# Optimization experiments

Hardware: AMD Instinct MI355X
Metric: run time of the kernel (lower is better)

## Reference

```python
import jax, jax.numpy as jnp
import numpy as np
from jax import lax

MAX_LEN = 40
SOS_ID = 2
VOCAB, EMB, HID, CTX = 32000, 512, 1024, 64
H2 = HID // 2
B, S = 256, 128


def gru_cell(x, h, wih, whh, bih, bhh):
    # PyTorch GRU equations: gates ordered (r, z, n)
    gx = x @ wih.T + bih
    gh = h @ whh.T + bhh
    rx, zx, nx = jnp.split(gx, 3, axis=-1)
    rh, zh, nh = jnp.split(gh, 3, axis=-1)
    r = jax.nn.sigmoid(rx + rh)
    z = jax.nn.sigmoid(zx + zh)
    n = jnp.tanh(nx + r * nh)
    return (1.0 - z) * n + z * h


def setup_inputs() -> dict:
    key = jax.random.key(0)
    ks = jax.random.split(key, 16)
    sd = 0.02
    emb_table = jax.random.normal(ks[0], (VOCAB, EMB), jnp.float32) * sd
    emb_table = emb_table.at[0].set(0.0)  # padding_idx=0
    def w(k, shape):
        return jax.random.normal(k, shape, jnp.float32) * sd
    inp = {
        "input_ids": jax.random.randint(ks[1], (B, S), 0, VOCAB),
        "context_vec": jax.random.normal(ks[2], (B, CTX), jnp.float32),
        "emb_table": emb_table,
        # encoder fwd direction
        "enc_wih_f": w(ks[3], (3 * H2, EMB)),
        "enc_whh_f": w(ks[4], (3 * H2, H2)),
        "enc_bih_f": w(ks[5], (3 * H2,)),
        "enc_bhh_f": w(ks[6], (3 * H2,)),
        # encoder bwd direction
        "enc_wih_b": w(ks[7], (3 * H2, EMB)),
        "enc_whh_b": w(ks[8], (3 * H2, H2)),
        "enc_bih_b": w(ks[9], (3 * H2,)),
        "enc_bhh_b": w(ks[10], (3 * H2,)),
        # decoder GRU: input = emb + hidden + context
        "dec_wih": w(ks[11], (3 * HID, EMB + HID + CTX)),
        "dec_whh": w(ks[12], (3 * HID, HID)),
        "dec_bih": w(ks[13], (3 * HID,)),
        "dec_bhh": w(ks[14], (3 * HID,)),
        "wout": w(ks[15], (VOCAB, HID)),
        "bout": jnp.zeros((VOCAB,), jnp.float32),
    }
    return inp


def reference(input_ids, context_vec, emb_table,
              enc_wih_f, enc_whh_f, enc_bih_f, enc_bhh_f,
              enc_wih_b, enc_whh_b, enc_bih_b, enc_bhh_b,
              dec_wih, dec_whh, dec_bih, dec_bhh, wout, bout):
    b = input_ids.shape[0]
    emb = emb_table[input_ids]                      # [B,S,E]
    emb_t = jnp.swapaxes(emb, 0, 1)                 # [S,B,E]

    def enc_f(h, x):
        return gru_cell(x, h, enc_wih_f, enc_whh_f, enc_bih_f, enc_bhh_f), None

    def enc_b(h, x):
        return gru_cell(x, h, enc_wih_b, enc_whh_b, enc_bih_b, enc_bhh_b), None

    h0 = jnp.zeros((b, H2), emb.dtype)
    hf, _ = lax.scan(enc_f, h0, emb_t)
    hb, _ = lax.scan(enc_b, h0, emb_t[::-1])
    # replicate torch's h_n.view(batch, -1) on a (2,B,H2) tensor (contiguous reshape)
    encoder_ctx = jnp.stack([hf, hb], axis=0).reshape(b, HID)   # [B,HID]

    ctx = jnp.concatenate([encoder_ctx, context_vec], axis=-1)  # [B,HID+CTX]
    h_dec0 = jnp.zeros((b, HID), emb.dtype)
    prev0 = jnp.full((b,), SOS_ID, dtype=jnp.int32)

    def dec_step(carry, _):
        h, prev = carry
        x = jnp.concatenate([emb_table[prev], ctx], axis=-1)
        h = gru_cell(x, h, dec_wih, dec_whh, dec_bih, dec_bhh)
        logits = h @ wout.T + bout                  # [B,V]
        probs = jax.nn.softmax(logits, axis=-1)
        nxt = jnp.argmax(probs, axis=-1).astype(jnp.int32)
        sel = jnp.take_along_axis(probs, nxt[:, None], axis=1)[:, 0]
        lp = jnp.log(sel + 1e-12)
        return (h, nxt), (nxt, lp)

    (_, _), (toks, lps) = lax.scan(dec_step, (h_dec0, prev0), None, length=MAX_LEN)
    return toks.T, lps.T   # [B,MAX_LEN] tokens, [B,MAX_LEN] log-probs
```

## Files before the change

kernel.cpp:

```cpp
#include <hip/hip_runtime.h>
#include <hip/hip_bf16.h>
#include <math.h>

#define B_    256
#define S_    128
#define EMB_  512
#define H2_   512
#define HID_  1024
#define CTX_  64
#define VOC_  32000
#define TMAX_ 40
#define SOS_  2

typedef unsigned short u16;
typedef __attribute__((ext_vector_type(8))) short short8;
typedef __attribute__((ext_vector_type(4))) float f32x4;

__device__ __forceinline__ float4 ld4(const float* p) {
    return *reinterpret_cast<const float4*>(p);
}
__device__ __forceinline__ float sigmoidf_(float x) { return 1.f / (1.f + expf(-x)); }
__device__ __forceinline__ u16 f2bf(float x) {
    union { float f; unsigned int u; } v; v.f = x;
    unsigned int r = v.u + 0x7FFFu + ((v.u >> 16) & 1u);
    return (u16)(r >> 16);
}
__device__ __forceinline__ unsigned pk2(float a, float b) {
    float2 t; t.x = a; t.y = b;
    __hip_bfloat162 h = __float22bfloat162_rn(t);
    return *reinterpret_cast<unsigned*>(&h);
}
__device__ __forceinline__ void merge_top2(float& v1, int& i1, float& v2, int& i2,
                                           float ov1, int oi1, float ov2, int oi2)
{
    if (ov1 > v1 || (ov1 == v1 && oi1 < i1)) {
        float tv = v1; int ti = i1;
        v1 = ov1; i1 = oi1;
        if (ov2 > tv || (ov2 == tv && oi2 < ti)) { v2 = ov2; i2 = oi2; }
        else                                     { v2 = tv;  i2 = ti;  }
    } else {
        if (ov1 > v2 || (ov1 == v2 && oi1 < i2)) { v2 = ov1; i2 = oi1; }
    }
}

template<int BM, int BN, int TM, int TN, int AMODE, int BGATHER, int BIASM>
__launch_bounds__(256)
__global__ void gemm_nt(const float* __restrict__ Ap,
                        const int*   __restrict__ ids,
                        const float* __restrict__ Ex,
                        const float* __restrict__ Bp, int ldb, int bofs,
                        const float* __restrict__ bias,
                        const float* __restrict__ addsrc,
                        float* __restrict__ Cp, int ldc,
                        int lda, int K, int s_base, int sdir)
{
    constexpr int BK = 32;
    __shared__ float As[BK][BM + 4];
    __shared__ float Bs[BK][BN + 4];
    const int t  = threadIdx.x;
    const int tx = t & 15, ty = t >> 4;
    const int m_base = blockIdx.y * BM;
    const int n_base = blockIdx.x * BN;

    float acc[TM][TN];
#pragma unroll
    for (int i = 0; i < TM; ++i)
#pragma unroll
        for (int j = 0; j < TN; ++j) acc[i][j] = 0.f;

    constexpr int A_PER = BM * BK / 4 / 256;
    constexpr int B_PER = BN * BK / 4 / 256;

    for (int k0 = 0; k0 < K; k0 += BK) {
#pragma unroll
        for (int j = 0; j < A_PER; ++j) {
            int f   = t + j * 256;
            int row = f >> 3;
            int kk  = (f & 7) << 2;
            int m   = m_base + row;
            float4 v;
            if constexpr (AMODE == 0) {
                v = ld4(Ap + (size_t)m * lda + k0 + kk);
            } else if constexpr (AMODE == 3) {
                int id = ids[m];
                v = ld4(Ex + (size_t)id * EMB_ + k0 + kk);
            } else {
                int k = k0 + kk;
                if (k < HID_) v = ld4(Ap + (size_t)m * HID_ + k);
                else          v = ld4(Ex + (size_t)m * CTX_ + (k - HID_));
            }
            As[kk + 0][row] = v.x; As[kk + 1][row] = v.y;
            As[kk + 2][row] = v.z; As[kk + 3][row] = v.w;
        }
#pragma unroll
        for (int j = 0; j < B_PER; ++j) {
            int f   = t + j * 256;
            int row = f >> 3;
            int kk  = (f & 7) << 2;
            float4 v;
            if constexpr (BGATHER == 1) {
                int n = n_base + row;
                int s = n >> 8, b = n & 255;
                int id = ids[b * S_ + s_base + sdir * s];
                v = ld4(Ex + (size_t)id * EMB_ + k0 + kk);
            } else {
                v = ld4(Bp + (size_t)(n_base + row) * ldb + bofs + k0 + kk);
            }
            Bs[kk + 0][row] = v.x; Bs[kk + 1][row] = v.y;
            Bs[kk + 2][row] = v.z; Bs[kk + 3][row] = v.w;
        }
        __syncthreads();
#pragma unroll
        for (int kk = 0; kk < BK; ++kk) {
            float a[TM], b[TN];
            *(float4*)&a[0] = ld4(&As[kk][ty * TM]);
            if constexpr (TM == 8) *(float4*)&a[4] = ld4(&As[kk][ty * TM + 4]);
            *(float4*)&b[0] = ld4(&Bs[kk][tx * TN]);
            if constexpr (TN == 8) *(float4*)&b[4] = ld4(&Bs[kk][tx * TN + 4]);
#pragma unroll
            for (int i = 0; i < TM; ++i)
#pragma unroll
                for (int j = 0; j < TN; ++j) acc[i][j] += a[i] * b[j];
        }
        __syncthreads();
    }
#pragma unroll
    for (int i = 0; i < TM; ++i) {
        int m = m_base + ty * TM + i;
#pragma unroll
        for (int j = 0; j < TN; ++j) {
            int n = n_base + tx * TN + j;
            float v = acc[i][j];
            if (bias) v += BIASM ? bias[m] : bias[n];
            if (addsrc) v += addsrc[(size_t)m * ldc + n];
            Cp[(size_t)m * ldc + n] = v;
        }
    }
}

__global__ void whh_trans(const float* __restrict__ whh_f, const float* __restrict__ whh_b,
                          float* __restrict__ whhX_f, float* __restrict__ whhX_b)
{
    int idx = blockIdx.x * 256 + threadIdx.x;
    const float* src = blockIdx.y ? whh_b : whh_f;
    float*       dst = blockIdx.y ? whhX_b : whhX_f;
    int k  = idx / 1536;
    int cc = idx - k * 1536;
    int u  = cc / 3;
    int g  = cc - u * 3;
    dst[idx] = src[(size_t)(g * 512 + u) * 512 + k];
}

#define RECBLK 128

union EncSM {
    struct { float hbuf[2][512][4]; float red[256][25]; } rec;
    struct { float As[32][132]; float Bs[32][132]; } gx;
};

__launch_bounds__(512)
__global__ void enc_fused(const float* __restrict__ grec_f, const float* __restrict__ grec_b,
                          float* __restrict__ gout_f, float* __restrict__ gout_b,
                          const float* __restrict__ whhX_f, const float* __restrict__ whhX_b,
                          const float* __restrict__ bhh_f, const float* __restrict__ bhh_b,
                          const float* __restrict__ wih_f, const float* __restrict__ wih_b,
                          const float* __restrict__ bih_f, const float* __restrict__ bih_b,
                          const int* __restrict__ ids, const float* __restrict__ emb,
                          float* __restrict__ hT, int do_rec, int gx_chunk, int nsteps)
{
    __shared__ __align__(16) EncSM sm;
    const int t = threadIdx.x;

    if (blockIdx.x >= RECBLK) {
        if (gx_chunk < 0) return;
        const int tt  = blockIdx.x - RECBLK;
        const int dz  = tt >= 192;
        const int t192 = dz ? tt - 192 : tt;
        const int m_base = (t192 & 15) * 128;
        const int n_base = (t192 >> 4) * 128;
        const float* W    = dz ? wih_b : wih_f;
        const float* bias = dz ? bih_b : bih_f;
        float*       Cp   = dz ? gout_b : gout_f;
        const int s_base  = dz ? (127 - 8 * gx_chunk) : (8 * gx_chunk);
        const int sdir    = dz ? -1 : 1;
        const int tx = t & 31, ty = t >> 5;

        float acc[8][4];
#pragma unroll
        for (int i = 0; i < 8; ++i)
#pragma unroll
            for (int j = 0; j < 4; ++j) acc[i][j] = 0.f;

        for (int k0 = 0; k0 < 512; k0 += 32) {
#pragma unroll
            for (int j = 0; j < 2; ++j) {
                int f   = t + j * 512;
                int row = f >> 3;
                int kk  = (f & 7) << 2;
                int m   = m_base + row;
                int s   = m >> 8, b = m & 255;
                int id  = ids[b * S_ + s_base + sdir * s];
                float4 v = ld4(emb + (size_t)id * EMB_ + k0 + kk);
                sm.gx.As[kk + 0][row] = v.x; sm.gx.As[kk + 1][row] = v.y;
                sm.gx.As[kk + 2][row] = v.z; sm.gx.As[kk + 3][row] = v.w;
                float4 wv = ld4(W + (size_t)(n_base + row) * 512 + k0 + kk);
                sm.gx.Bs[kk + 0][row] = wv.x; sm.gx.Bs[kk + 1][row] = wv.y;
                sm.gx.Bs[kk + 2][row] = wv.z; sm.gx.Bs[kk + 3][row] = wv.w;
            }
            __syncthreads();
#pragma unroll
            for (int kk = 0; kk < 32; ++kk) {
                float a[8], b[4];
                *(float4*)&a[0] = ld4(&sm.gx.As[kk][ty * 8]);
                *(float4*)&a[4] = ld4(&sm.gx.As[kk][ty * 8 + 4]);
                *(float4*)&b[0] = ld4(&sm.gx.Bs[kk][tx * 4]);
#pragma unroll
                for (int i = 0; i < 8; ++i)
#pragma unroll
                    for (int j = 0; j < 4; ++j) acc[i][j] += a[i] * b[j];
            }
            __syncthreads();
        }
#pragma unroll
        for (int i = 0; i < 8; ++i) {
            int m = m_base + ty * 8 + i;
#pragma unroll
            for (int j = 0; j < 4; ++j) {
                int n = n_base + tx * 4 + j;
                Cp[(size_t)m * 1536 + n] = acc[i][j] + bias[n];
            }
        }
        return;
    }

    if (!do_rec) return;
    const int bid = blockIdx.x;
    const int xcd = bid & 7;
    const int dir = xcd >> 2;
    const int local = (bid >> 3) * 4 + (xcd & 3);
    const int r0 = local * 4;
    const float* gx  = dir ? grec_b : grec_f;
    const float* whx = dir ? whhX_b : whhX_f;
    const float* bhh = dir ? bhh_b : bhh_f;
    float* hTd = hT + (size_t)dir * (256 * 512);

    const int kh = t >> 8;
    const int tu = t & 255;
    const int k_base = kh << 8;

    for (int i = t; i < 2048; i += 512) {
        int r = i >> 9, u = i & 511;
        sm.rec.hbuf[0][u][r] = hTd[(size_t)(r0 + r) * 512 + u];
    }
    float bh[2][3];
#pragma unroll
    for (int uu = 0; uu < 2; ++uu)
#pragma unroll
        for (int g = 0; g < 3; ++g)
            bh[uu][g] = bhh[g * 512 + tu * 2 + uu];
    __syncthreads();

    for (int st = 0; st < nsteps; ++st) {
        const int cur = st & 1, nxt = cur ^ 1;

        float2 gxv[3][4];
        if (!kh) {
#pragma unroll
            for (int g = 0; g < 3; ++g)
#pragma unroll
                for (int r = 0; r < 4; ++r)
                    gxv[g][r] = *(const float2*)&gx[(size_t)((st << 8) + r0 + r) * 1536
                                                    + (g << 9) + (tu << 1)];
        }

        float acc[2][3][4];
#pragma unroll
        for (int uu = 0; uu < 2; ++uu)
#pragma unroll
            for (int g = 0; g < 3; ++g)
#pragma unroll
                for (int r = 0; r < 4; ++r) acc[uu][g][r] = 0.f;

        const float* wp = whx + (size_t)k_base * 1536 + tu * 6;
#pragma unroll 4
        for (int kk = 0; kk < 256; ++kk) {
            float4 hv = *(const float4*)&sm.rec.hbuf[cur][k_base + kk][0];
            float2 w0 = *(const float2*)(wp + 0);
            float2 w1 = *(const float2*)(wp + 2);
            float2 w2 = *(const float2*)(wp + 4);
            const float* hvp = (const float*)&hv;
#pragma unroll
            for (int r = 0; r < 4; ++r) {
                float h = hvp[r];
                acc[0][0][r] += w0.x * h;
                acc[0][1][r] += w0.y * h;
                acc[0][2][r] += w1.x * h;
                acc[1][0][r] += w1.y * h;
                acc[1][1][r] += w2.x * h;
                acc[1][2][r] += w2.y * h;
            }
            wp += 1536;
        }

        if (kh) {
#pragma unroll
            for (int uu = 0; uu < 2; ++uu)
#pragma unroll
                for (int g = 0; g < 3; ++g)
#pragma unroll
                    for (int r = 0; r < 4; ++r)
                        sm.rec.red[tu][(uu * 3 + g) * 4 + r] = acc[uu][g][r];
        }
        __syncthreads();
        if (!kh) {
#pragma unroll
            for (int uu = 0; uu < 2; ++uu)
#pragma unroll
                for (int g = 0; g < 3; ++g)
#pragma unroll
                    for (int r = 0; r < 4; ++r)
                        acc[uu][g][r] += sm.rec.red[tu][(uu * 3 + g) * 4 + r];
#pragma unroll
            for (int uu = 0; uu < 2; ++uu) {
                int u = tu * 2 + uu;
#pragma unroll
                for (int r = 0; r < 4; ++r) {
                    float gr = uu ? gxv[0][r].y : gxv[0][r].x;
                    float gz = uu ? gxv[1][r].y : gxv[1][r].x;
                    float gn = uu ? gxv[2][r].y : gxv[2][r].x;
                    float hold = sm.rec.hbuf[cur][u][r];
                    float rg = sigmoidf_(gr + acc[uu][0][r] + bh[uu][0]);
                    float zg = sigmoidf_(gz + acc[uu][1][r] + bh[uu][1]);
                    float ng = tanhf(gn + rg * (acc[uu][2][r] + bh[uu][2]));
                    sm.rec.hbuf[nxt][u][r] = (1.f - zg) * ng + zg * hold;
                }
            }
        }
        __syncthreads();
    }

    const int lb = nsteps & 1;
    for (int i = t; i < 2048; i += 512) {
        int r = i >> 9, u = i & 511;
        hTd[(size_t)(r0 + r) * 512 + u] = sm.rec.hbuf[lb][u][r];
    }
}

__global__ void zerof(float* __restrict__ p, int n)
{
    int i = blockIdx.x * 256 + threadIdx.x;
    if (i < n) p[i] = 0.f;
}

__global__ void init_dec(float* __restrict__ hdec, u16* __restrict__ hbf, int* __restrict__ prev)
{
    int i = blockIdx.x * 256 + threadIdx.x;
    hdec[i] = 0.f; hbf[i] = 0;
    if (i < B_) prev[i] = SOS_;
}

__global__ void hcat_build(const float* __restrict__ hT, float* __restrict__ hcat)
{
    int idx = blockIdx.x * 256 + threadIdx.x;
    int b = idx >> 10, k = idx & 1023;
    int d = b >> 7;
    int rr = ((2 * b) & 255) + (k >> 9);
    int kk = k & 511;
    hcat[idx] = hT[(size_t)d * 131072 + (size_t)rr * 512 + kk];
}

__launch_bounds__(256)
__global__ void dec_gemm2(const float* __restrict__ hdec, const int* __restrict__ prev,
                          const float* __restrict__ emb,
                          const float* __restrict__ dwhh, const float* __restrict__ dwih,
                          const float* __restrict__ dbhh, const float* __restrict__ gctx,
                          float* __restrict__ ghbuf, float* __restrict__ gibuf)
{
    constexpr int BK = 32;
    __shared__ float As[BK][68];
    __shared__ float Bs[BK][68];
    const int t  = threadIdx.x;
    const int tx = t & 15, ty = t >> 4;
    const bool isH = blockIdx.y < 4;
    const int m_base = (isH ? blockIdx.y : (blockIdx.y - 4)) * 64;
    const int n_base = blockIdx.x * 64;
    const int K   = isH ? 1024 : 512;
    const float* Bp = isH ? dwhh : dwih;
    const int ldb  = isH ? 1024 : 1600;
    float* Cp = isH ? ghbuf : gibuf;

    float acc[4][4];
#pragma unroll
    for (int i = 0; i < 4; ++i)
#pragma unroll
        for (int j = 0; j < 4; ++j) acc[i][j] = 0.f;

    for (int k0 = 0; k0 < K; k0 += BK) {
#pragma unroll
        for (int j = 0; j < 2; ++j) {
            int f   = t + j * 256;
            int row = f >> 3;
            int kk  = (f & 7) << 2;
            int m   = m_base + row;
            float4 v;
            if (isH) v = ld4(hdec + (size_t)m * HID_ + k0 + kk);
            else     v = ld4(emb + (size_t)prev[m] * EMB_ + k0 + kk);
            As[kk + 0][row] = v.x; As[kk + 1][row] = v.y;
            As[kk + 2][row] = v.z; As[kk + 3][row] = v.w;
            float4 w = ld4(Bp + (size_t)(n_base + row) * ldb + k0 + kk);
            Bs[kk + 0][row] = w.x; Bs[kk + 1][row] = w.y;
            Bs[kk + 2][row] = w.z; Bs[kk + 3][row] = w.w;
        }
        __syncthreads();
#pragma unroll
        for (int kk = 0; kk < BK; ++kk) {
            float a[4], b[4];
            *(float4*)&a[0] = ld4(&As[kk][ty * 4]);
            *(float4*)&b[0] = ld4(&Bs[kk][tx * 4]);
#pragma unroll
            for (int i = 0; i < 4; ++i)
#pragma unroll
                for (int j = 0; j < 4; ++j) acc[i][j] += a[i] * b[j];
        }
        __syncthreads();
    }
#pragma unroll
    for (int i = 0; i < 4; ++i) {
        int m = m_base + ty * 4 + i;
#pragma unroll
        for (int j = 0; j < 4; ++j) {
            int n = n_base + tx * 4 + j;
            float v = acc[i][j];
            if (isH) v += dbhh[n];
            else     v += gctx[(size_t)m * 3072 + n];
            Cp[(size_t)m * 3072 + n] = v;
        }
    }
}

__global__ void dec_combine(const float* __restrict__ gi, const float* __restrict__ gh,
                            float* __restrict__ hdec, u16* __restrict__ hbf)
{
    int idx = blockIdx.x * 256 + threadIdx.x;
    int b = idx >> 10, u = idx & 1023;
    size_t gb = (size_t)b * 3072;
    float r = sigmoidf_(gi[gb + u]            + gh[gb + u]);
    float z = sigmoidf_(gi[gb + HID_ + u]     + gh[gb + HID_ + u]);
    float n = tanhf    (gi[gb + 2 * HID_ + u] + r * gh[gb + 2 * HID_ + u]);
    float v = (1.f - z) * n + z * hdec[idx];
    hdec[idx] = v;
    hbf[idx] = f2bf(v);
}

__launch_bounds__(512)
__global__ void gemm_logits(const u16* __restrict__ A, const float* __restrict__ Wf,
                            const float* __restrict__ bias,
                            float* __restrict__ pmax, float* __restrict__ psum,
                            float* __restrict__ ptv, int* __restrict__ pti)
{
    __shared__ u16 As[256][72];
    __shared__ u16 Bs[128][72];
    const int t = threadIdx.x;
    const int lane = t & 63, wave = t >> 6;
    const int wm = (wave & 3) * 64, wn = (wave >> 2) * 64;
    const int n0 = blockIdx.x * 128;
    f32x4 acc[4][4];
#pragma unroll
    for (int i = 0; i < 4; ++i)
#pragma unroll
        for (int j = 0; j < 4; ++j) acc[i][j] = (f32x4){0.f, 0.f, 0.f, 0.f};
    const int arow = t >> 1, aoff = (t & 1) * 32;
    const int brow = t >> 2, boff = (t & 3) * 16;

    for (int k0 = 0; k0 < 1024; k0 += 64) {
#pragma unroll
        for (int q = 0; q < 4; ++q) {
            *(uint4*)&As[arow][aoff + q * 8] =
                *(const uint4*)(A + (size_t)arow * 1024 + k0 + aoff + q * 8);
        }
        const float* wr = Wf + (size_t)(n0 + brow) * 1024 + k0 + boff;
#pragma unroll
        for (int q = 0; q < 2; ++q) {
            float4 x = ld4(wr + q * 8);
            float4 y = ld4(wr + q * 8 + 4);
            uint4 o;
            o.x = pk2(x.x, x.y); o.y = pk2(x.z, x.w);
            o.z = pk2(y.x, y.y); o.w = pk2(y.z, y.w);
            *(uint4*)&Bs[brow][boff + q * 8] = o;
        }
        __syncthreads();
#pragma unroll
        for (int s = 0; s < 2; ++s) {
            short8 a[4], b[4];
            int j0 = s * 32 + (lane >> 4) * 8;
#pragma unroll
            for (int i = 0; i < 4; ++i) {
                a[i] = *(const short8*)&As[wm + i * 16 + (lane & 15)][j0];
                b[i] = *(const short8*)&Bs[wn + i * 16 + (lane & 15)][j0];
            }
#pragma unroll
            for (int i = 0; i < 4; ++i)
#pragma unroll
                for (int j = 0; j < 4; ++j)
                    acc[i][j] = __builtin_amdgcn_mfma_f32_16x16x32_bf16(a[i], b[j], acc[i][j], 0, 0, 0);
        }
        __syncthreads();
    }

    const int htile = blockIdx.x * 2 + (wn >> 6);
    float bn[4]; int jx[4];
#pragma unroll
    for (int j = 0; j < 4; ++j) { jx[j] = n0 + wn + j * 16 + (lane & 15); bn[j] = bias[jx[j]]; }
#pragma unroll
    for (int i = 0; i < 4; ++i) {
#pragma unroll
        for (int rr = 0; rr < 4; ++rr) {
            float v[4];
#pragma unroll
            for (int j = 0; j < 4; ++j) v[j] = acc[i][j][rr] + bn[j];
            float v1 = v[0], v2 = -3.4e38f; int i1 = jx[0], i2 = 0x7fffffff;
#pragma unroll
            for (int j = 1; j < 4; ++j) {
                if (v[j] > v1)      { v2 = v1; i2 = i1; v1 = v[j]; i1 = jx[j]; }
                else if (v[j] > v2) { v2 = v[j]; i2 = jx[j]; }
            }
#pragma unroll
            for (int mask = 1; mask <= 8; mask <<= 1) {
                float ov1 = __shfl_xor(v1, mask), ov2 = __shfl_xor(v2, mask);
                int   oi1 = __shfl_xor(i1, mask), oi2 = __shfl_xor(i2, mask);
                merge_top2(v1, i1, v2, i2, ov1, oi1, ov2, oi2);
            }
            float rmax = v1;
            float s = 0.f;
#pragma unroll
            for (int j = 0; j < 4; ++j) s += expf(v[j] - rmax);
#pragma unroll
            for (int mask = 1; mask <= 8; mask <<= 1) s += __shfl_xor(s, mask);
            if ((lane & 15) == 0) {
                int row = wm + i * 16 + (lane >> 4) * 4 + rr;
                size_t base = (size_t)row * 500 + htile;
                pmax[base] = rmax; psum[base] = s;
                ptv[base * 2] = v1; ptv[base * 2 + 1] = v2;
                pti[base * 2] = i1; pti[base * 2 + 1] = i2;
            }
        }
    }
}

__launch_bounds__(256)
__global__ void dec_reduce(const float* __restrict__ pmax, const float* __restrict__ psum,
                           const float* __restrict__ ptv, const int* __restrict__ pti,
                           const float* __restrict__ hdec, const float* __restrict__ wout,
                           const float* __restrict__ bout,
                           float* __restrict__ out, int* __restrict__ prev, int tstep)
{
    __shared__ float sv[256]; __shared__ int sti[256]; __shared__ int ssl[256];
    __shared__ float cvv[1000]; __shared__ int cii[1000];
    __shared__ float c8v[8]; __shared__ int c8i[8]; __shared__ float c8e[8];
    const int b = blockIdx.x, tid = threadIdx.x;
    const float* pm = pmax + (size_t)b * 500;
    const float* ps = psum + (size_t)b * 500;

    float m = -3.4e38f;
    for (int i = tid; i < 500; i += 256) m = fmaxf(m, pm[i]);
    sv[tid] = m; __syncthreads();
    for (int off = 128; off; off >>= 1) { if (tid < off) sv[tid] = fmaxf(sv[tid], sv[tid + off]); __syncthreads(); }
    float gmax = sv[0]; __syncthreads();

    float s = 0.f;
    for (int i = tid; i < 500; i += 256) s += ps[i] * expf(pm[i] - gmax);
    sv[tid] = s; __syncthreads();
    for (int off = 128; off; off >>= 1) { if (tid < off) sv[tid] += sv[tid + off]; __syncthreads(); }
    float gsum = sv[0]; __syncthreads();

    for (int i = tid; i < 1000; i += 256) { cvv[i] = ptv[(size_t)b * 1000 + i]; cii[i] = pti[(size_t)b * 1000 + i]; }
    __syncthreads();

    for (int c = 0; c < 8; ++c) {
        float bv = -3.4e38f; int bi = 0x7fffffff, bs = 0;
        for (int i = tid; i < 1000; i += 256) {
            float v = cvv[i]; int ix = cii[i];
            if (v > bv || (v == bv && ix < bi)) { bv = v; bi = ix; bs = i; }
        }
        sv[tid] = bv; sti[tid] = bi; ssl[tid] = bs; __syncthreads();
        for (int off = 128; off; off >>= 1) {
            if (tid < off) {
                if (sv[tid + off] > sv[tid] ||
                    (sv[tid + off] == sv[tid] && sti[tid + off] < sti[tid])) {
                    sv[tid] = sv[tid + off]; sti[tid] = sti[tid + off]; ssl[tid] = ssl[tid + off];
                }
            }
            __syncthreads();
        }
        if (tid == 0) { c8v[c] = sv[0]; c8i[c] = sti[0]; cvv[ssl[0]] = -3.4e38f; }
        __syncthreads();
    }

    {
        int lane = tid & 63, wv = tid >> 6;
        const float* hr = hdec + (size_t)b * HID_;
        for (int c = wv; c < 8; c += 4) {
            const float* wr = wout + (size_t)c8i[c] * HID_;
            float a = 0.f;
            for (int k = lane * 4; k < HID_; k += 256) {
                float4 x = ld4(hr + k), y = ld4(wr + k);
                a += x.x * y.x + x.y * y.y + x.z * y.z + x.w * y.w;
            }
#pragma unroll
            for (int off = 32; off; off >>= 1) a += __shfl_down(a, off);
            if (lane == 0) c8e[c] = a + bout[c8i[c]];
        }
    }
    __syncthreads();

    if (tid == 0) {
        float bv = c8e[0]; int bi = c8i[0]; float av = c8v[0];
        for (int c = 1; c < 8; ++c)
            if (c8e[c] > bv || (c8e[c] == bv && c8i[c] < bi)) { bv = c8e[c]; bi = c8i[c]; av = c8v[c]; }
        float p = expf(av - gmax) / gsum;
        float lp = logf(p + 1e-12f);
        out[(size_t)b * TMAX_ + tstep] = (float)bi;
        out[B_ * TMAX_ + (size_t)b * TMAX_ + tstep] = lp;
        prev[b] = bi;
    }
}

extern "C" void kernel_launch(void* const* d_in, const int* in_sizes, int n_in,
                              void* d_out, int out_size, void* d_ws, size_t ws_size,
                              hipStream_t stream)
{
    const int*   ids   = (const int*)  d_in[0];
    const float* cvec  = (const float*)d_in[1];
    const float* emb   = (const float*)d_in[2];
    const float* wih_f = (const float*)d_in[3];
    const float* whh_f = (const float*)d_in[4];
    const float* bih_f = (const float*)d_in[5];
    const float* bhh_f = (const float*)d_in[6];
    const float* wih_b = (const float*)d_in[7];
    const float* whh_b = (const float*)d_in[8];
    const float* bih_b = (const float*)d_in[9];
    const float* bhh_b = (const float*)d_in[10];
    const float* dwih  = (const float*)d_in[11];
    const float* dwhh  = (const float*)d_in[12];
    const float* dbih  = (const float*)d_in[13];
    const float* dbhh  = (const float*)d_in[14];
    const float* wout  = (const float*)d_in[15];
    const float* bout  = (const float*)d_in[16];
    float* out = (float*)d_out;

    float* w      = (float*)d_ws;
    float* buf0_f = w;
    float* buf0_b = w + 3145728;
    float* buf1_f = w + 6291456;
    float* buf1_b = w + 9437184;
    float* hT     = w + 12582912;
    float* hcat   = w + 12845056;
    float* hdec   = w + 13107200;
    float* gctx   = w + 13369344;
    u16*   hdecb  = (u16*)(w + 14155776);
    int*   prev   = (int*)(w + 14286848);
    float* whhX_f = w + 14287104;
    float* whhX_b = w + 15073536;
    float* gibuf  = buf0_f;
    float* ghbuf  = buf0_f + 786432;
    float* pmax   = buf0_f + 1572864;
    float* psum   = buf0_f + 1700864;
    float* ptv    = buf0_f + 1828864;
    int*   pti    = (int*)(buf0_f + 2084864);

    zerof<<<1024, 256, 0, stream>>>(hT, 262144);
    init_dec<<<1024, 256, 0, stream>>>(hdec, hdecb, prev);
    whh_trans<<<dim3(3072, 2), 256, 0, stream>>>(whh_f, whh_b, whhX_f, whhX_b);

    enc_fused<<<512, 512, 0, stream>>>(
        buf0_f, buf0_b, buf0_f, buf0_b, whhX_f, whhX_b, bhh_f, bhh_b,
        wih_f, wih_b, bih_f, bih_b, ids, emb, hT, 0, 0, 8);
    for (int c = 1; c < 16; ++c) {
        float* rf = ((c - 1) & 1) ? buf1_f : buf0_f;
        float* rb = ((c - 1) & 1) ? buf1_b : buf0_b;
        float* of = (c & 1) ? buf1_f : buf0_f;
        float* ob = (c & 1) ? buf1_b : buf0_b;
        enc_fused<<<512, 512, 0, stream>>>(
            rf, rb, of, ob, whhX_f, whhX_b, bhh_f, bhh_b,
            wih_f, wih_b, bih_f, bih_b, ids, emb, hT, 1, c, 8);
    }
    enc_fused<<<512, 512, 0, stream>>>(
        buf1_f, buf1_b, buf1_f, buf1_b, whhX_f, whhX_b, bhh_f, bhh_b,
        wih_f, wih_b, bih_f, bih_b, ids, emb, hT, 1, -1, 8);

    hcat_build<<<1024, 256, 0, stream>>>(hT, hcat);

    gemm_nt<64, 64, 4, 4, 2, 0, 0><<<dim3(48, 4), 256, 0, stream>>>(
        hcat, nullptr, cvec, dwih, 1600, 512, dbih, nullptr,
        gctx, 3072, 1024, 1088, 0, 0);

    for (int t = 0; t < TMAX_; ++t) {
        dec_gemm2<<<dim3(48, 8), 256, 0, stream>>>(
            hdec, prev, emb, dwhh, dwih, dbhh, gctx, ghbuf, gibuf);
        dec_combine<<<1024, 256, 0, stream>>>(gibuf, ghbuf, hdec, hdecb);
        gemm_logits<<<dim3(250, 1), 512, 0, stream>>>(hdecb, wout, bout,
                                                      pmax, psum, ptv, pti);
        dec_reduce<<<256, 256, 0, stream>>>(pmax, psum, ptv, pti,
                                            hdec, wout, bout, out, prev, t);
    }
}
```

Measured before the change: 10.65 ms.

## Fuse decoder GRU gemms with gate combine, pre-convert wout to bf16, simplify encoder recurrence

The decoder's two gate gemms and the separate combine kernel become a single dec_step kernel. It uses gate-interleaved transposed weights so each block computes r/z/n for its own units and writes the new hidden state directly, with ping-pong hidden buffers. The output projection weights are converted to bf16 once, when workspace allows, so the logits gemm no longer converts fp32 each step. The encoder recurrence drops its two-way K split and shared-memory reduction, and each thread now handles one unit over the full K. That cuts a sync and a reduction, but each thread runs a longer serial loop and the decoder launches only 128 blocks.

```diff
diff --git a/kernel.cpp b/kernel.cpp
--- a/kernel.cpp
+++ b/kernel.cpp
@@ -139,29 +139,52 @@
 }
 
 __global__ void whh_trans(const float* __restrict__ whh_f, const float* __restrict__ whh_b,
-                          float* __restrict__ whhX_f, float* __restrict__ whhX_b)
+                          float* __restrict__ whhU_f, float* __restrict__ whhU_b)
 {
     int idx = blockIdx.x * 256 + threadIdx.x;
     const float* src = blockIdx.y ? whh_b : whh_f;
-    float*       dst = blockIdx.y ? whhX_b : whhX_f;
+    float*       dst = blockIdx.y ? whhU_b : whhU_f;
     int k  = idx / 1536;
-    int cc = idx - k * 1536;
-    int u  = cc / 3;
-    int g  = cc - u * 3;
+    int rem = idx - k * 1536;
+    int g  = rem >> 9;
+    int u  = rem & 511;
     dst[idx] = src[(size_t)(g * 512 + u) * 512 + k];
 }
 
+__global__ void dec_wtrans(const float* __restrict__ dwhh, const float* __restrict__ dwih,
+                           float* __restrict__ dwX, float* __restrict__ dwiX)
+{
+    int idx = blockIdx.x * 256 + threadIdx.x;
+    if (blockIdx.y == 0) {
+        int c = idx >> 10, k = idx & 1023;
+        int u = c / 3, g = c - u * 3;
+        dwX[idx] = dwhh[(size_t)(g * 1024 + u) * 1024 + k];
+    } else {
+        if (idx >= 1572864) return;
+        int c = idx >> 9, k = idx & 511;
+        int u = c / 3, g = c - u * 3;
+        dwiX[idx] = dwih[(size_t)(g * 1024 + u) * 1600 + k];
+    }
+}
+
+__global__ void wbf_conv(const float* __restrict__ wout, unsigned* __restrict__ wbf)
+{
+    int idx = blockIdx.x * 256 + threadIdx.x;
+    float2 v = *reinterpret_cast<const float2*>(wout + (size_t)idx * 2);
+    wbf[idx] = pk2(v.x, v.y);
+}
+
 #define RECBLK 128
 
 union EncSM {
-    struct { float hbuf[2][512][4]; float red[256][25]; } rec;
+    struct { float hbuf[2][512][4]; } rec;
     struct { float As[32][132]; float Bs[32][132]; } gx;
 };
 
 __launch_bounds__(512)
 __global__ void enc_fused(const float* __restrict__ grec_f, const float* __restrict__ grec_b,
                           float* __restrict__ gout_f, float* __restrict__ gout_b,
-                          const float* __restrict__ whhX_f, const float* __restrict__ whhX_b,
+                          const float* __restrict__ whhU_f, const float* __restrict__ whhU_b,
                           const float* __restrict__ bhh_f, const float* __restrict__ bhh_b,
                           const float* __restrict__ wih_f, const float* __restrict__ wih_b,
                           const float* __restrict__ bih_f, const float* __restrict__ bih_b,
@@ -240,110 +263,63 @@
     const int local = (bid >> 3) * 4 + (xcd & 3);
     const int r0 = local * 4;
     const float* gx  = dir ? grec_b : grec_f;
-    const float* whx = dir ? whhX_b : whhX_f;
+    const float* whx = dir ? whhU_b : whhU_f;
     const float* bhh = dir ? bhh_b : bhh_f;
     float* hTd = hT + (size_t)dir * (256 * 512);
 
-    const int kh = t >> 8;
-    const int tu = t & 255;
-    const int k_base = kh << 8;
-
-    for (int i = t; i < 2048; i += 512) {
-        int r = i >> 9, u = i & 511;
+    const int u = t;
+
+#pragma unroll
+    for (int r = 0; r < 4; ++r)
         sm.rec.hbuf[0][u][r] = hTd[(size_t)(r0 + r) * 512 + u];
-    }
-    float bh[2][3];
-#pragma unroll
-    for (int uu = 0; uu < 2; ++uu)
-#pragma unroll
-        for (int g = 0; g < 3; ++g)
-            bh[uu][g] = bhh[g * 512 + tu * 2 + uu];
+    const float bh0 = bhh[u], bh1 = bhh[512 + u], bh2 = bhh[1024 + u];
     __syncthreads();
 
     for (int st = 0; st < nsteps; ++st) {
         const int cur = st & 1, nxt = cur ^ 1;
 
-        float2 gxv[3][4];
-        if (!kh) {
-#pragma unroll
-            for (int g = 0; g < 3; ++g)
-#pragma unroll
-                for (int r = 0; r < 4; ++r)
-                    gxv[g][r] = *(const float2*)&gx[(size_t)((st << 8) + r0 + r) * 1536
-                                                    + (g << 9) + (tu << 1)];
-        }
-
-        float acc[2][3][4];
-#pragma unroll
-        for (int uu = 0; uu < 2; ++uu)
-#pragma unroll
-            for (int g = 0; g < 3; ++g)
-#pragma unroll
-                for (int r = 0; r < 4; ++r) acc[uu][g][r] = 0.f;
-
-        const float* wp = whx + (size_t)k_base * 1536 + tu * 6;
-#pragma unroll 4
-        for (int kk = 0; kk < 256; ++kk) {
-            float4 hv = *(const float4*)&sm.rec.hbuf[cur][k_base + kk][0];
-            float2 w0 = *(const float2*)(wp + 0);
-            float2 w1 = *(const float2*)(wp + 2);
-            float2 w2 = *(const float2*)(wp + 4);
+        float gx0[4], gx1[4], gx2[4];
+#pragma unroll
+        for (int r = 0; r < 4; ++r) {
+            size_t base = (size_t)((st << 8) + r0 + r) * 1536 + u;
+            gx0[r] = gx[base];
+            gx1[r] = gx[base + 512];
+            gx2[r] = gx[base + 1024];
+        }
+
+        float acc0[4] = {0.f,0.f,0.f,0.f};
+        float acc1[4] = {0.f,0.f,0.f,0.f};
+        float acc2[4] = {0.f,0.f,0.f,0.f};
+        const float* wp = whx + u;
+#pragma unroll 8
+        for (int kk = 0; kk < 512; ++kk) {
+            float4 hv = *(const float4*)&sm.rec.hbuf[cur][kk][0];
+            float w0 = wp[0], w1 = wp[512], w2 = wp[1024];
             const float* hvp = (const float*)&hv;
 #pragma unroll
             for (int r = 0; r < 4; ++r) {
-                float h = hvp[r];
-                acc[0][0][r] += w0.x * h;
-                acc[0][1][r] += w0.y * h;
-                acc[0][2][r] += w1.x * h;
-                acc[1][0][r] += w1.y * h;
-                acc[1][1][r] += w2.x * h;
-                acc[1][2][r] += w2.y * h;
+                acc0[r] += w0 * hvp[r];
+                acc1[r] += w1 * hvp[r];
+                acc2[r] += w2 * hvp[r];
             }
             wp += 1536;
         }
 
-        if (kh) {
-#pragma unroll
-            for (int uu = 0; uu < 2; ++uu)
-#pragma unroll
-                for (int g = 0; g < 3; ++g)
-#pragma unroll
-                    for (int r = 0; r < 4; ++r)
-                        sm.rec.red[tu][(uu * 3 + g) * 4 + r] = acc[uu][g][r];
-        }
-        __syncthreads();
-        if (!kh) {
-#pragma unroll
-            for (int uu = 0; uu < 2; ++uu)
-#pragma unroll
-                for (int g = 0; g < 3; ++g)
-#pragma unroll
-                    for (int r = 0; r < 4; ++r)
-                        acc[uu][g][r] += sm.rec.red[tu][(uu * 3 + g) * 4 + r];
-#pragma unroll
-            for (int uu = 0; uu < 2; ++uu) {
-                int u = tu * 2 + uu;
-#pragma unroll
-                for (int r = 0; r < 4; ++r) {
-                    float gr = uu ? gxv[0][r].y : gxv[0][r].x;
-                    float gz = uu ? gxv[1][r].y : gxv[1][r].x;
-                    float gn = uu ? gxv[2][r].y : gxv[2][r].x;
-                    float hold = sm.rec.hbuf[cur][u][r];
-                    float rg = sigmoidf_(gr + acc[uu][0][r] + bh[uu][0]);
-                    float zg = sigmoidf_(gz + acc[uu][1][r] + bh[uu][1]);
-                    float ng = tanhf(gn + rg * (acc[uu][2][r] + bh[uu][2]));
-                    sm.rec.hbuf[nxt][u][r] = (1.f - zg) * ng + zg * hold;
-                }
-            }
+#pragma unroll
+        for (int r = 0; r < 4; ++r) {
+            float hold = sm.rec.hbuf[cur][u][r];
+            float rg = sigmoidf_(gx0[r] + acc0[r] + bh0);
+            float zg = sigmoidf_(gx1[r] + acc1[r] + bh1);
+            float ng = tanhf(gx2[r] + rg * (acc2[r] + bh2));
+            sm.rec.hbuf[nxt][u][r] = (1.f - zg) * ng + zg * hold;
         }
         __syncthreads();
     }
 
     const int lb = nsteps & 1;
-    for (int i = t; i < 2048; i += 512) {
-        int r = i >> 9, u = i & 511;
+#pragma unroll
+    for (int r = 0; r < 4; ++r)
         hTd[(size_t)(r0 + r) * 512 + u] = sm.rec.hbuf[lb][u][r];
-    }
 }
 
 __global__ void zerof(float* __restrict__ p, int n)
@@ -370,90 +346,123 @@
 }
 
 __launch_bounds__(256)
-__global__ void dec_gemm2(const float* __restrict__ hdec, const int* __restrict__ prev,
-                          const float* __restrict__ emb,
-                          const float* __restrict__ dwhh, const float* __restrict__ dwih,
-                          const float* __restrict__ dbhh, const float* __restrict__ gctx,
-                          float* __restrict__ ghbuf, float* __restrict__ gibuf)
-{
-    constexpr int BK = 32;
-    __shared__ float As[BK][68];
-    __shared__ float Bs[BK][68];
+__global__ void dec_step(const float* __restrict__ hin, const int* __restrict__ prev,
+                         const float* __restrict__ emb,
+                         const float* __restrict__ dwX, const float* __restrict__ dwiX,
+                         const float* __restrict__ dbhh, const float* __restrict__ gctx,
+                         float* __restrict__ hout, u16* __restrict__ hbf)
+{
+    __shared__ float As[32][68];
+    __shared__ float Bs[32][100];
     const int t  = threadIdx.x;
     const int tx = t & 15, ty = t >> 4;
-    const bool isH = blockIdx.y < 4;
-    const int m_base = (isH ? blockIdx.y : (blockIdx.y - 4)) * 64;
-    const int n_base = blockIdx.x * 64;
-    const int K   = isH ? 1024 : 512;
-    const float* Bp = isH ? dwhh : dwih;
-    const int ldb  = isH ? 1024 : 1600;
-    float* Cp = isH ? ghbuf : gibuf;
-
-    float acc[4][4];
+    const int ublk = blockIdx.x * 32;
+    const int c0   = blockIdx.x * 96;
+    const int m0   = blockIdx.y * 64;
+
+    float accH[4][6], accI[4][6];
 #pragma unroll
     for (int i = 0; i < 4; ++i)
 #pragma unroll
-        for (int j = 0; j < 4; ++j) acc[i][j] = 0.f;
-
-    for (int k0 = 0; k0 < K; k0 += BK) {
+        for (int j = 0; j < 6; ++j) { accH[i][j] = 0.f; accI[i][j] = 0.f; }
+
+    for (int k0 = 0; k0 < 1024; k0 += 32) {
 #pragma unroll
         for (int j = 0; j < 2; ++j) {
             int f   = t + j * 256;
             int row = f >> 3;
             int kk  = (f & 7) << 2;
-            int m   = m_base + row;
-            float4 v;
-            if (isH) v = ld4(hdec + (size_t)m * HID_ + k0 + kk);
-            else     v = ld4(emb + (size_t)prev[m] * EMB_ + k0 + kk);
+            float4 v = ld4(hin + (size_t)(m0 + row) * HID_ + k0 + kk);
             As[kk + 0][row] = v.x; As[kk + 1][row] = v.y;
             As[kk + 2][row] = v.z; As[kk + 3][row] = v.w;
-            float4 w = ld4(Bp + (size_t)(n_base + row) * ldb + k0 + kk);
-            Bs[kk + 0][row] = w.x; Bs[kk + 1][row] = w.y;
-            Bs[kk + 2][row] = w.z; Bs[kk + 3][row] = w.w;
-        }
-        __syncthreads();
-#pragma unroll
-        for (int kk = 0; kk < BK; ++kk) {
-            float a[4], b[4];
+        }
+#pragma unroll
+        for (int j = 0; j < 3; ++j) {
+            int f   = t + j * 256;
+            int row = f >> 3;
+            int kk  = (f & 7) << 2;
+            float4 v = ld4(dwX + (size_t)(c0 + row) * 1024 + k0 + kk);
+            Bs[kk + 0][row] = v.x; Bs[kk + 1][row] = v.y;
+            Bs[kk + 2][row] = v.z; Bs[kk + 3][row] = v.w;
+        }
+        __syncthreads();
+#pragma unroll
+        for (int kk = 0; kk < 32; ++kk) {
+            float a[4], b[6];
             *(float4*)&a[0] = ld4(&As[kk][ty * 4]);
-            *(float4*)&b[0] = ld4(&Bs[kk][tx * 4]);
+            *(float2*)&b[0] = *(const float2*)&Bs[kk][tx * 6];
+            *(float2*)&b[2] = *(const float2*)&Bs[kk][tx * 6 + 2];
+            *(float2*)&b[4] = *(const float2*)&Bs[kk][tx * 6 + 4];
 #pragma unroll
             for (int i = 0; i < 4; ++i)
 #pragma unroll
-                for (int j = 0; j < 4; ++j) acc[i][j] += a[i] * b[j];
-        }
-        __syncthreads();
-    }
+                for (int j = 0; j < 6; ++j) accH[i][j] += a[i] * b[j];
+        }
+        __syncthreads();
+    }
+
+    for (int k0 = 0; k0 < 512; k0 += 32) {
+#pragma unroll
+        for (int j = 0; j < 2; ++j) {
+            int f   = t + j * 256;
+            int row = f >> 3;
+            int kk  = (f & 7) << 2;
+            int id  = prev[m0 + row];
+            float4 v = ld4(emb + (size_t)id * EMB_ + k0 + kk);
+            As[kk + 0][row] = v.x; As[kk + 1][row] = v.y;
+            As[kk + 2][row] = v.z; As[kk + 3][row] = v.w;
+        }
+#pragma unroll
+        for (int j = 0; j < 3; ++j) {
+            int f   = t + j * 256;
+            int row = f >> 3;
+            int kk  = (f & 7) << 2;
+            float4 v = ld4(dwiX + (size_t)(c0 + row) * 512 + k0 + kk);
+            Bs[kk + 0][row] = v.x; Bs[kk + 1][row] = v.y;
+            Bs[kk + 2][row] = v.z; Bs[kk + 3][row] = v.w;
+        }
+        __syncthreads();
+#pragma unroll
+        for (int kk = 0; kk < 32; ++kk) {
+            float a[4], b[6];
+            *(float4*)&a[0] = ld4(&As[kk][ty * 4]);
+            *(float2*)&b[0] = *(const float2*)&Bs[kk][tx * 6];
+            *(float2*)&b[2] = *(const float2*)&Bs[kk][tx * 6 + 2];
+            *(float2*)&b[4] = *(const float2*)&Bs[kk][tx * 6 + 4];
+#pragma unroll
+            for (int i = 0; i < 4; ++i)
+#pragma unroll
+                for (int j = 0; j < 6; ++j) accI[i][j] += a[i] * b[j];
+        }
+        __syncthreads();
+    }
+
 #pragma unroll
     for (int i = 0; i < 4; ++i) {
-        int m = m_base + ty * 4 + i;
-#pragma unroll
-        for (int j = 0; j < 4; ++j) {
-            int n = n_base + tx * 4 + j;
-            float v = acc[i][j];
-            if (isH) v += dbhh[n];
-            else     v += gctx[(size_t)m * 3072 + n];
-            Cp[(size_t)m * 3072 + n] = v;
-        }
-    }
-}
-
-__global__ void dec_combine(const float* __restrict__ gi, const float* __restrict__ gh,
-                            float* __restrict__ hdec, u16* __restrict__ hbf)
-{
-    int idx = blockIdx.x * 256 + threadIdx.x;
-    int b = idx >> 10, u = idx & 1023;
-    size_t gb = (size_t)b * 3072;
-    float r = sigmoidf_(gi[gb + u]            + gh[gb + u]);
-    float z = sigmoidf_(gi[gb + HID_ + u]     + gh[gb + HID_ + u]);
-    float n = tanhf    (gi[gb + 2 * HID_ + u] + r * gh[gb + 2 * HID_ + u]);
-    float v = (1.f - z) * n + z * hdec[idx];
-    hdec[idx] = v;
-    hbf[idx] = f2bf(v);
+        int m = m0 + ty * 4 + i;
+#pragma unroll
+        for (int ul = 0; ul < 2; ++ul) {
+            int u = ublk + tx * 2 + ul;
+            float gir = accI[i][ul * 3 + 0] + gctx[(size_t)m * 3072 + u];
+            float giz = accI[i][ul * 3 + 1] + gctx[(size_t)m * 3072 + 1024 + u];
+            float gin = accI[i][ul * 3 + 2] + gctx[(size_t)m * 3072 + 2048 + u];
+            float ghr = accH[i][ul * 3 + 0] + dbhh[u];
+            float ghz = accH[i][ul * 3 + 1] + dbhh[1024 + u];
+            float ghn = accH[i][ul * 3 + 2] + dbhh[2048 + u];
+            float r = sigmoidf_(gir + ghr);
+            float z = sigmoidf_(giz + ghz);
+            float n = tanhf(gin + r * ghn);
+            float hold = hin[(size_t)m * HID_ + u];
+            float v = (1.f - z) * n + z * hold;
+            hout[(size_t)m * HID_ + u] = v;
+            hbf[(size_t)m * HID_ + u] = f2bf(v);
+        }
+    }
 }
 
 __launch_bounds__(512)
 __global__ void gemm_logits(const u16* __restrict__ A, const float* __restrict__ Wf,
+                            const u16* __restrict__ Wbf,
                             const float* __restrict__ bias,
                             float* __restrict__ pmax, float* __restrict__ psum,
                             float* __restrict__ ptv, int* __restrict__ pti)
@@ -478,15 +487,21 @@
             *(uint4*)&As[arow][aoff + q * 8] =
                 *(const uint4*)(A + (size_t)arow * 1024 + k0 + aoff + q * 8);
         }
-        const float* wr = Wf + (size_t)(n0 + brow) * 1024 + k0 + boff;
-#pragma unroll
-        for (int q = 0; q < 2; ++q) {
-            float4 x = ld4(wr + q * 8);
-            float4 y = ld4(wr + q * 8 + 4);
-            uint4 o;
-            o.x = pk2(x.x, x.y); o.y = pk2(x.z, x.w);
-            o.z = pk2(y.x, y.y); o.w = pk2(y.z, y.w);
-            *(uint4*)&Bs[brow][boff + q * 8] = o;
+        if (Wbf) {
+            const u16* wr = Wbf + (size_t)(n0 + brow) * 1024 + k0 + boff;
+            *(uint4*)&Bs[brow][boff]     = *(const uint4*)(wr);
+            *(uint4*)&Bs[brow][boff + 8] = *(const uint4*)(wr + 8);
+        } else {
+            const float* wr = Wf + (size_t)(n0 + brow) * 1024 + k0 + boff;
+#pragma unroll
+            for (int q = 0; q < 2; ++q) {
+                float4 x = ld4(wr + q * 8);
+                float4 y = ld4(wr + q * 8 + 4);
+                uint4 o;
+                o.x = pk2(x.x, x.y); o.y = pk2(x.z, x.w);
+                o.z = pk2(y.x, y.y); o.w = pk2(y.z, y.w);
+                *(uint4*)&Bs[brow][boff + q * 8] = o;
+            }
         }
         __syncthreads();
 #pragma unroll
@@ -655,25 +670,28 @@
     float* buf1_b = w + 9437184;
     float* hT     = w + 12582912;
     float* hcat   = w + 12845056;
-    float* hdec   = w + 13107200;
+    float* hdecA  = w + 13107200;
     float* gctx   = w + 13369344;
     u16*   hdecb  = (u16*)(w + 14155776);
     int*   prev   = (int*)(w + 14286848);
-    float* whhX_f = w + 14287104;
-    float* whhX_b = w + 15073536;
-    float* gibuf  = buf0_f;
-    float* ghbuf  = buf0_f + 786432;
-    float* pmax   = buf0_f + 1572864;
-    float* psum   = buf0_f + 1700864;
-    float* ptv    = buf0_f + 1828864;
-    int*   pti    = (int*)(buf0_f + 2084864);
+    float* whhU_f = w + 14287104;
+    float* whhU_b = w + 15073536;
+    u16*   wbf    = (u16*)(w + 15859968);
+    const int use_wbf = (ws_size >= (size_t)(15859968 + 16384000) * 4);
+    float* dwX    = buf0_f;
+    float* dwiX   = buf0_f + 3145728;
+    float* pmax   = buf1_f;
+    float* psum   = buf1_f + 128000;
+    float* ptv    = buf1_f + 256000;
+    int*   pti    = (int*)(buf1_f + 512000);
+    float* hdecB  = buf1_f + 768000;
 
     zerof<<<1024, 256, 0, stream>>>(hT, 262144);
-    init_dec<<<1024, 256, 0, stream>>>(hdec, hdecb, prev);
-    whh_trans<<<dim3(3072, 2), 256, 0, stream>>>(whh_f, whh_b, whhX_f, whhX_b);
+    init_dec<<<1024, 256, 0, stream>>>(hdecA, hdecb, prev);
+    whh_trans<<<dim3(3072, 2), 256, 0, stream>>>(whh_f, whh_b, whhU_f, whhU_b);
 
     enc_fused<<<512, 512, 0, stream>>>(
-        buf0_f, buf0_b, buf0_f, buf0_b, whhX_f, whhX_b, bhh_f, bhh_b,
+        buf0_f, buf0_b, buf0_f, buf0_b, whhU_f, whhU_b, bhh_f, bhh_b,
         wih_f, wih_b, bih_f, bih_b, ids, emb, hT, 0, 0, 8);
     for (int c = 1; c < 16; ++c) {
         float* rf = ((c - 1) & 1) ? buf1_f : buf0_f;
@@ -681,26 +699,33 @@
         float* of = (c & 1) ? buf1_f : buf0_f;
         float* ob = (c & 1) ? buf1_b : buf0_b;
         enc_fused<<<512, 512, 0, stream>>>(
-            rf, rb, of, ob, whhX_f, whhX_b, bhh_f, bhh_b,
+            rf, rb, of, ob, whhU_f, whhU_b, bhh_f, bhh_b,
             wih_f, wih_b, bih_f, bih_b, ids, emb, hT, 1, c, 8);
     }
     enc_fused<<<512, 512, 0, stream>>>(
-        buf1_f, buf1_b, buf1_f, buf1_b, whhX_f, whhX_b, bhh_f, bhh_b,
+        buf1_f, buf1_b, buf1_f, buf1_b, whhU_f, whhU_b, bhh_f, bhh_b,
         wih_f, wih_b, bih_f, bih_b, ids, emb, hT, 1, -1, 8);
 
     hcat_build<<<1024, 256, 0, stream>>>(hT, hcat);
+
+    dec_wtrans<<<dim3(12288, 2), 256, 0, stream>>>(dwhh, dwih, dwX, dwiX);
+    if (use_wbf)
+        wbf_conv<<<64000, 256, 0, stream>>>(wout, (unsigned*)wbf);
 
     gemm_nt<64, 64, 4, 4, 2, 0, 0><<<dim3(48, 4), 256, 0, stream>>>(
         hcat, nullptr, cvec, dwih, 1600, 512, dbih, nullptr,
         gctx, 3072, 1024, 1088, 0, 0);
 
+    float* hin = hdecA;
+    float* hout = hdecB;
     for (int t = 0; t < TMAX_; ++t) {
-        dec_gemm2<<<dim3(48, 8), 256, 0, stream>>>(
-            hdec, prev, emb, dwhh, dwih, dbhh, gctx, ghbuf, gibuf);
-        dec_combine<<<1024, 256, 0, stream>>>(gibuf, ghbuf, hdec, hdecb);
-        gemm_logits<<<dim3(250, 1), 512, 0, stream>>>(hdecb, wout, bout,
-                                                      pmax, psum, ptv, pti);
+        dec_step<<<dim3(32, 4), 256, 0, stream>>>(
+            hin, prev, emb, dwX, dwiX, dbhh, gctx, hout, hdecb);
+        gemm_logits<<<dim3(250, 1), 512, 0, stream>>>(
+            hdecb, wout, use_wbf ? wbf : (const u16*)nullptr, bout,
+            pmax, psum, ptv, pti);
         dec_reduce<<<256, 256, 0, stream>>>(pmax, psum, ptv, pti,
-                                            hdec, wout, bout, out, prev, t);
-    }
-}
+                                            hout, wout, bout, out, prev, t);
+        float* tmp = hin; hin = hout; hout = tmp;
+    }
+}
```

Measured after the change: 12.50 ms. 1.17x slower.
